# Performance work log

Measured on AMD Instinct MI355X. Metric: run time of the kernel, lower is better.

Reference implementation:

```python
import jax, jax.numpy as jnp
import numpy as np

N_NODES = 50000
N_EDGES = 500000
IN_CH = 128
OUT_CH = 64
HEADS = 4


def setup_inputs() -> dict:
    key = jax.random.key(0)
    ks = jax.random.split(key, 9)
    x = jax.random.normal(ks[0], (N_NODES, IN_CH), dtype=jnp.float32)
    edge_index = jax.random.randint(ks[1], (2, N_EDGES), 0, N_NODES, dtype=jnp.int64)
    edge_weights = jax.random.uniform(ks[2], (N_EDGES, 1), dtype=jnp.float32)
    # xavier-uniform params, stored as [in, out] so y = x @ W
    def xavier(k, shape):
        fan_in, fan_out = shape
        lim = float(np.sqrt(6.0 / (fan_in + fan_out)))
        return jax.random.uniform(k, shape, minval=-lim, maxval=lim, dtype=jnp.float32)
    Wq = xavier(ks[3], (IN_CH, OUT_CH * HEADS))
    Wk = xavier(ks[4], (IN_CH, OUT_CH * HEADS))
    Wv = xavier(ks[5], (IN_CH, OUT_CH * HEADS))
    We = xavier(ks[6], (1, HEADS))
    Wout = xavier(ks[7], (OUT_CH * HEADS, OUT_CH))
    b_out = jnp.zeros((OUT_CH,), dtype=jnp.float32)
    return {"x": x, "edge_index": edge_index, "edge_weights": edge_weights,
            "Wq": Wq, "Wk": Wk, "Wv": Wv, "We": We, "Wout": Wout, "b_out": b_out}


def reference(x, edge_index, edge_weights, Wq, Wk, Wv, We, Wout, b_out):
    num_nodes = x.shape[0]
    src = edge_index[0]
    tgt = edge_index[1]
    x_src = x[src]                                    # [E, in]
    x_tgt = x[tgt]                                    # [E, in]
    q = (x_tgt @ Wq).reshape(-1, HEADS, OUT_CH)       # [E, H, C]
    k = (x_src @ Wk).reshape(-1, HEADS, OUT_CH)
    v = (x_src @ Wv).reshape(-1, HEADS, OUT_CH)
    attn = jnp.sum(q * k, axis=-1) / jnp.sqrt(jnp.float32(OUT_CH))  # [E, H]
    attn = attn + edge_weights @ We                   # [E, H]
    attn = jax.nn.leaky_relu(attn, negative_slope=0.2)
    attn = jax.nn.softmax(attn, axis=0)               # global softmax over edges (as in source)
    weighted_v = attn[..., None] * v                  # [E, H, C]
    out = jax.ops.segment_sum(weighted_v, tgt, num_segments=num_nodes)  # [N, H, C]
    out = out.reshape(num_nodes, HEADS * OUT_CH) @ Wout + b_out         # [N, out]
    if x.shape == out.shape:
        out = out + x
    return out
```

## Files before the change

### kernel.cpp

```cpp
#include <hip/hip_runtime.h>
#include <hip/hip_bf16.h>
#include <hip/hip_fp16.h>

#define N_NODES 50000
#define N_EDGES 500000
#define IN_CH   128
#define D       256
#define UDIM    512
#define OUT_CH  64
#define HEADS   4
#define NC      49
#define PCAP    448
#define DEPTH   4

#define NB_X16  6250
#define NB_HIST 1954
#define NB_MB   256
#define NB_ZB   128
#define NB_GEMM 1564
#define NB_SCAT 1954
#define NB_K4   (NB_GEMM + NB_SCAT)

typedef _Float16 half8 __attribute__((ext_vector_type(8)));
typedef _Float16 half2_t __attribute__((ext_vector_type(2)));
typedef float   floatx4 __attribute__((ext_vector_type(4)));

typedef __attribute__((address_space(1))) const void as1_void;
typedef __attribute__((address_space(3))) void as3_void;

__device__ __forceinline__ void gll16(const void* g, void* l) {
    __builtin_amdgcn_global_load_lds((as1_void*)g, (as3_void*)l, 16, 0, 0);
}

__device__ __forceinline__ float dpp_xor1(float x) {
    return __int_as_float(__builtin_amdgcn_mov_dpp(__float_as_int(x), 0xB1, 0xf, 0xf, true));
}
__device__ __forceinline__ float dpp_xor2(float x) {
    return __int_as_float(__builtin_amdgcn_mov_dpp(__float_as_int(x), 0x4E, 0xf, 0xf, true));
}

__global__ __launch_bounds__(256) void k1_prep_kernel(const float* __restrict__ x,
                                                      __half* __restrict__ x16,
                                                      const int* __restrict__ ei,
                                                      int* __restrict__ cnt,
                                                      double* __restrict__ S,
                                                      const float* __restrict__ Wq,
                                                      const float* __restrict__ Wk,
                                                      const float* __restrict__ Wv,
                                                      const float* __restrict__ Wout,
                                                      __half* __restrict__ M16t,
                                                      __half* __restrict__ Zc16t) {
    __shared__ float sbuf[4][64];
    const int b = blockIdx.x, tid = threadIdx.x;
    if (b < NB_X16) {
        int i = b * 256 + tid;
        if (i < HEADS) S[i] = 0.0;
        int k = i * 4;
        if (k < N_NODES * IN_CH) {
            float4 v = *(const float4*)(x + k);
            union { __half2 h[2]; uint2 u; } pk;
            pk.h[0] = __floats2half2_rn(v.x, v.y);
            pk.h[1] = __floats2half2_rn(v.z, v.w);
            *(uint2*)(x16 + k) = pk.u;
        }
    } else if (b < NB_X16 + NB_HIST) {
        int e = (b - NB_X16) * 256 + tid;
        if (e < N_EDGES) atomicAdd(&cnt[ei[N_EDGES + e]], 1);
    } else if (b < NB_X16 + NB_HIST + NB_MB) {
        const int r = (b - NB_X16 - NB_HIST) * 2 + (tid >> 7);
        const int i = tid & 127;
        const int h = r >> 7, j = r & 127;
        float* buf = sbuf[tid >> 7];
        if (i < 64) buf[i] = Wk[(size_t)j * D + h * 64 + i];
        __syncthreads();
        const float4* qr = (const float4*)(Wq + (size_t)i * D + h * 64);
        float s = 0.f;
        #pragma unroll
        for (int c4 = 0; c4 < 16; ++c4) {
            float4 q = qr[c4];
            s += q.x * buf[c4 * 4] + q.y * buf[c4 * 4 + 1]
               + q.z * buf[c4 * 4 + 2] + q.w * buf[c4 * 4 + 3];
        }
        M16t[(size_t)r * IN_CH + i] = __float2half(s);
    } else {
        const int r = (b - NB_X16 - NB_HIST - NB_MB) * 4 + (tid >> 6);
        const int c = tid & 63;
        const int h = r >> 7, i = r & 127;
        float* buf = sbuf[tid >> 6];
        buf[c] = Wv[(size_t)i * D + h * 64 + c];
        __syncthreads();
        float s = 0.f;
        #pragma unroll 8
        for (int j = 0; j < 64; ++j)
            s += buf[j] * Wout[(size_t)(h * 64 + j) * OUT_CH + c];
        Zc16t[(size_t)c * UDIM + r] = __float2half(s);
    }
}

__global__ __launch_bounds__(256) void k2_scan_reduce_kernel(const int* __restrict__ cnt,
                                                             int* __restrict__ csum) {
    const int b = blockIdx.x, tid = threadIdx.x;
    const int lane = tid & 63, wid = tid >> 6;
    int s = 0;
    int idx0 = b * 1024 + tid * 4;
    #pragma unroll
    for (int i = 0; i < 4; ++i) {
        int idx = idx0 + i;
        if (idx < N_NODES) s += cnt[idx];
    }
    #pragma unroll
    for (int m = 1; m < 64; m <<= 1) s += __shfl_xor(s, m, 64);
    __shared__ int w4[4];
    if (lane == 0) w4[wid] = s;
    __syncthreads();
    if (tid == 0) csum[b] = w4[0] + w4[1] + w4[2] + w4[3];
}

__global__ __launch_bounds__(256) void k3_scan_chunks_kernel(int* __restrict__ cnt,
                                                             const int* __restrict__ csum,
                                                             int* __restrict__ rp) {
    __shared__ int stop[64];
    __shared__ int wsum[4];
    const int b = blockIdx.x, tid = threadIdx.x;
    const int lane = tid & 63, wid = tid >> 6;
    if (tid < 64) stop[tid] = (tid < NC) ? csum[tid] : 0;
    __syncthreads();
    int base = 0;
    for (int w = 0; w < b; ++w) base += stop[w];
    int v[4];
    const int idx0 = b * 1024 + tid * 4;
    #pragma unroll
    for (int i = 0; i < 4; ++i) {
        int idx = idx0 + i;
        v[i] = (idx < N_NODES) ? cnt[idx] : 0;
    }
    int tsum = v[0] + v[1] + v[2] + v[3];
    int x = tsum;
    #pragma unroll
    for (int d = 1; d < 64; d <<= 1) {
        int y = __shfl_up(x, d, 64);
        if (lane >= d) x += y;
    }
    if (lane == 63) wsum[wid] = x;
    __syncthreads();
    int woff = 0;
    for (int w = 0; w < wid; ++w) woff += wsum[w];
    int excl = base + woff + x - tsum;
    #pragma unroll
    for (int i = 0; i < 4; ++i) {
        int idx = idx0 + i;
        if (idx < N_NODES) { rp[idx] = excl; cnt[idx] = excl; }
        excl += v[i];
    }
}

__global__ __launch_bounds__(256) void k4_gemmu_scatter_kernel(const __half* __restrict__ x16,
                                                               const __half* __restrict__ M16t,
                                                               __half* __restrict__ u16,
                                                               const int* __restrict__ ei,
                                                               const float* __restrict__ ew,
                                                               int* __restrict__ cnt,
                                                               int2* __restrict__ payload) {
    __shared__ __half Bm[128][136];
    const int tid = threadIdx.x;
    const int b = blockIdx.x;
    const int glo = (int)(((long long)b * NB_GEMM) / NB_K4);
    const int ghi = (int)(((long long)(b + 1) * NB_GEMM) / NB_K4);
    if (ghi == glo) {
        int e = (b - glo) * 256 + tid;
        if (e < N_EDGES) {
            int s = ei[e], t = ei[N_EDGES + e];
            int pos = atomicAdd(&cnt[t], 1);
            payload[pos] = make_int2(s, __float_as_int(ew[e]));
        }
        return;
    }
    const int m0 = (glo % 391) * 128;
    const int colbase = (glo / 391) * 128;
    {
        const int r = tid >> 1, part = tid & 1;
        const uint4* sb = (const uint4*)(M16t + (size_t)(colbase + r) * IN_CH + part * 64);
        uint4* db = (uint4*)&Bm[r][part * 64];
        #pragma unroll
        for (int q = 0; q < 8; ++q) db[q] = sb[q];
    }

    const int w = tid >> 6, lane = tid & 63;
    const int mrow = lane & 15, quad = lane >> 4;

    half8 a[2][4];
    #pragma unroll
    for (int mt = 0; mt < 2; ++mt) {
        int row = min(m0 + w * 32 + mt * 16 + mrow, N_NODES - 1);
        const __half* ab = x16 + (size_t)row * IN_CH + quad * 8;
        #pragma unroll
        for (int ks = 0; ks < 4; ++ks) a[mt][ks] = *(const half8*)(ab + ks * 32);
    }
    __syncthreads();

    floatx4 acc[2][8];
    #pragma unroll
    for (int mt = 0; mt < 2; ++mt)
        #pragma unroll
        for (int nt = 0; nt < 8; ++nt)
            acc[mt][nt] = (floatx4){0.f, 0.f, 0.f, 0.f};

    #pragma unroll
    for (int nt = 0; nt < 8; ++nt) {
        #pragma unroll
        for (int ks = 0; ks < 4; ++ks) {
            half8 bfr = *(const half8*)&Bm[nt * 16 + mrow][ks * 32 + quad * 8];
            acc[0][nt] = __builtin_amdgcn_mfma_f32_16x16x32_f16(a[0][ks], bfr, acc[0][nt], 0, 0, 0);
            acc[1][nt] = __builtin_amdgcn_mfma_f32_16x16x32_f16(a[1][ks], bfr, acc[1][nt], 0, 0, 0);
        }
    }
    __syncthreads();
    #pragma unroll
    for (int mt = 0; mt < 2; ++mt)
        #pragma unroll
        for (int nt = 0; nt < 8; ++nt)
            #pragma unroll
            for (int r = 0; r < 4; ++r)
                Bm[w * 32 + mt * 16 + quad * 4 + r][nt * 16 + mrow] = __float2half(acc[mt][nt][r]);
    __syncthreads();
    {
        const int r = tid >> 1, part = tid & 1;
        if (m0 + r < N_NODES) {
            const uint4* s4 = (const uint4*)&Bm[r][part * 64];
            uint4* d4 = (uint4*)(u16 + (size_t)(m0 + r) * UDIM + colbase + part * 64);
            #pragma unroll
            for (int q = 0; q < 8; ++q) d4[q] = s4[q];
        }
    }
}

__global__ __launch_bounds__(256) void edge_fused_kernel(const __half* __restrict__ u16,
                                                         const __half* __restrict__ x16,
                                                         const int* __restrict__ rp,
                                                         const int* __restrict__ cnt,
                                                         const int2* __restrict__ payload,
                                                         const float* __restrict__ We,
                                                         __half* __restrict__ y16,
                                                         double* __restrict__ S) {
    __shared__ __half xring[4][DEPTH][512];
    __shared__ int2 pbuf[PCAP];
    __shared__ float sblk[4];
    const int tid = threadIdx.x;
    const int nodebase = blockIdx.x * 16;

    const int span0 = rp[nodebase];
    const int span1 = cnt[nodebase + 15];
    const int span  = span1 - span0;
    const int span_len = min(span, PCAP);
    for (int i = tid; i < span_len; i += 256) pbuf[i] = payload[span0 + i];
    if (tid < 4) sblk[tid] = 0.f;
    __syncthreads();

    const int w = tid >> 6, lane = tid & 63;
    const int g = lane >> 4;
    const int l16 = lane & 15;
    const int h = l16 >> 2;
    const int q = l16 & 3;
    const int node = nodebase + (tid >> 4);
    const float wev = We[h];

    uint4 ur4[4];
    {
        const uint4* ub = (const uint4*)(u16 + (size_t)node * UDIM + h * 128 + q * 32);
        ur4[0] = ub[0]; ur4[1] = ub[1]; ur4[2] = ub[2]; ur4[3] = ub[3];
    }
    const half2_t* uh = (const half2_t*)ur4;

    half2_t yacc[16];
    #pragma unroll
    for (int t = 0; t < 16; ++t) yacc[t] = (half2_t){(_Float16)0.f, (_Float16)0.f};

    float sacc = 0.f;
    const int start = rp[node];
    const int end = cnt[node];
    const int ng = end - start;

    if (span <= PCAP) {
        int nmax = ng;
        nmax = max(nmax, __shfl_xor(nmax, 16, 64));
        nmax = max(nmax, __shfl_xor(nmax, 32, 64));
        if (nmax > 0) {
            const int chunk_off = (l16 ^ g) * 8;
            auto src_of = [&](int t) -> const __half* {
                int idx = min(start + t, end - 1);
                idx = max(idx, span0);
                int s = pbuf[idx - span0].x;
                return x16 + (size_t)s * IN_CH + chunk_off;
            };
            #pragma unroll
            for (int s = 0; s < DEPTH; ++s)
                gll16(src_of(s), &xring[w][s][0]);

            for (int t = 0; t < nmax; ++t) {
                const int slot = t & (DEPTH - 1);
                asm volatile("s_waitcnt vmcnt(3)" ::: "memory");
                __builtin_amdgcn_sched_barrier(0);
                const uint4* rb = (const uint4*)&xring[w][slot][g * 128 + q * 32];
                uint4 xr0 = rb[0 ^ g];
                uint4 xr1 = rb[1 ^ g];
                uint4 xr2 = rb[2 ^ g];
                uint4 xr3 = rb[3 ^ g];
                asm volatile("s_waitcnt lgkmcnt(0)" ::: "memory");
                __builtin_amdgcn_sched_barrier(0);
                gll16(src_of(t + DEPTH), &xring[w][slot][0]);

                int2 pl;
                {
                    int idx = min(start + t, end - 1);
                    idx = max(idx, span0);
                    pl = pbuf[idx - span0];
                }
                uint4 xr[4] = {xr0, xr1, xr2, xr3};
                const half2_t* xh = (const half2_t*)xr;
                float d0 = 0.f, d1 = 0.f, d2 = 0.f, d3 = 0.f;
                #pragma unroll
                for (int tt = 0; tt < 4; ++tt) {
                    d0 = __builtin_amdgcn_fdot2(uh[tt],      xh[tt],      d0, false);
                    d1 = __builtin_amdgcn_fdot2(uh[tt + 4],  xh[tt + 4],  d1, false);
                    d2 = __builtin_amdgcn_fdot2(uh[tt + 8],  xh[tt + 8],  d2, false);
                    d3 = __builtin_amdgcn_fdot2(uh[tt + 12], xh[tt + 12], d3, false);
                }
                float dot = (d0 + d1) + (d2 + d3);
                dot += dpp_xor1(dot);
                dot += dpp_xor2(dot);
                float l = dot * 0.125f + __int_as_float(pl.y) * wev;
                l = fmaxf(l, 0.2f * l);
                float p = __expf(l);
                if (t < ng) {
                    if (q == 0) sacc += p;
                    half2_t p2 = (half2_t){(_Float16)p, (_Float16)p};
                    #pragma unroll
                    for (int tt = 0; tt < 16; ++tt)
                        yacc[tt] = p2 * xh[tt] + yacc[tt];
                }
            }
        }
    } else {
        auto getpl = [&](int e) -> int2 {
            int idx = e - span0;
            return (idx < PCAP) ? pbuf[idx] : payload[e];
        };
        int2 pl = make_int2(0, 0);
        uint4 xr[4];
        if (start < end) {
            pl = getpl(start);
            const uint4* xb = (const uint4*)(x16 + (size_t)pl.x * IN_CH + q * 32);
            xr[0] = xb[0]; xr[1] = xb[1]; xr[2] = xb[2]; xr[3] = xb[3];
        }
        for (int e = start; e < end; ++e) {
            int2 pln = pl;
            uint4 xrn[4] = {xr[0], xr[1], xr[2], xr[3]};
            if (e + 1 < end) {
                pln = getpl(e + 1);
                const uint4* xb = (const uint4*)(x16 + (size_t)pln.x * IN_CH + q * 32);
                xrn[0] = xb[0]; xrn[1] = xb[1]; xrn[2] = xb[2]; xrn[3] = xb[3];
            }
            const half2_t* xh = (const half2_t*)xr;
            float dot = 0.f;
            #pragma unroll
            for (int t = 0; t < 16; ++t)
                dot = __builtin_amdgcn_fdot2(uh[t], xh[t], dot, false);
            dot += __shfl_xor(dot, 1, 16);
            dot += __shfl_xor(dot, 2, 16);
            float l = dot * 0.125f + __int_as_float(pl.y) * wev;
            l = fmaxf(l, 0.2f * l);
            float p = __expf(l);
            if (q == 0) sacc += p;
            half2_t p2 = (half2_t){(_Float16)p, (_Float16)p};
            #pragma unroll
            for (int t = 0; t < 16; ++t)
                yacc[t] = p2 * xh[t] + yacc[t];
            pl = pln;
            xr[0] = xrn[0]; xr[1] = xrn[1]; xr[2] = xrn[2]; xr[3] = xrn[3];
        }
    }
    {
        uint4* yo = (uint4*)(y16 + (size_t)node * UDIM + h * 128 + q * 32);
        const uint4* ys = (const uint4*)yacc;
        yo[0] = ys[0]; yo[1] = ys[1]; yo[2] = ys[2]; yo[3] = ys[3];
    }
    __syncthreads();
    if (q == 0) atomicAdd(&sblk[h], sacc);
    __syncthreads();
    if (tid < 4) atomicAdd(&S[tid], (double)sblk[tid]);
}

__global__ __launch_bounds__(256) void gemm_out_mfma_kernel(const __half* __restrict__ y16,
                                                            const __half* __restrict__ Zc16t,
                                                            const double* __restrict__ S,
                                                            const float* __restrict__ b_out,
                                                            float* __restrict__ out) {
    __shared__ __half Ay[128][136];
    __shared__ __half Bz[64][136];
    __shared__ float invs_s[4];
    const int m0 = blockIdx.x * 128;
    const int tid = threadIdx.x;
    if (tid < 4) invs_s[tid] = (float)(1.0 / S[tid]);

    const int w = tid >> 6, lane = tid & 63;
    const int mrow = lane & 15, quad = lane >> 4;

    floatx4 result[2][4];
    #pragma unroll
    for (int mt = 0; mt < 2; ++mt)
        #pragma unroll
        for (int nt = 0; nt < 4; ++nt)
            result[mt][nt] = (floatx4){0.f, 0.f, 0.f, 0.f};

    for (int h = 0; h < HEADS; ++h) {
        {
            const int r = tid >> 1, part = tid & 1;
            uint4 va[8];
            if (m0 + r < N_NODES) {
                const uint4* src = (const uint4*)(y16 + (size_t)(m0 + r) * UDIM + h * 128 + part * 64);
                #pragma unroll
                for (int qq = 0; qq < 8; ++qq) va[qq] = src[qq];
            } else {
                #pragma unroll
                for (int qq = 0; qq < 8; ++qq) va[qq] = make_uint4(0u, 0u, 0u, 0u);
            }
            uint4* da = (uint4*)&Ay[r][part * 64];
            #pragma unroll
            for (int qq = 0; qq < 8; ++qq) da[qq] = va[qq];
        }
        {
            const int r = tid >> 2, part = tid & 3;
            const uint4* sb = (const uint4*)(Zc16t + (size_t)r * UDIM + h * 128 + part * 32);
            uint4* db = (uint4*)&Bz[r][part * 32];
            #pragma unroll
            for (int qq = 0; qq < 4; ++qq) db[qq] = sb[qq];
        }
        __syncthreads();

        half8 a[2][4];
        #pragma unroll
        for (int mt = 0; mt < 2; ++mt)
            #pragma unroll
            for (int ks = 0; ks < 4; ++ks)
                a[mt][ks] = *(const half8*)&Ay[w * 32 + mt * 16 + mrow][ks * 32 + quad * 8];

        floatx4 acc[2][4];
        #pragma unroll
        for (int mt = 0; mt < 2; ++mt)
            #pragma unroll
            for (int nt = 0; nt < 4; ++nt)
                acc[mt][nt] = (floatx4){0.f, 0.f, 0.f, 0.f};

        #pragma unroll
        for (int nt = 0; nt < 4; ++nt) {
            #pragma unroll
            for (int ks = 0; ks < 4; ++ks) {
                half8 bfr = *(const half8*)&Bz[nt * 16 + mrow][ks * 32 + quad * 8];
                acc[0][nt] = __builtin_amdgcn_mfma_f32_16x16x32_f16(a[0][ks], bfr, acc[0][nt], 0, 0, 0);
                acc[1][nt] = __builtin_amdgcn_mfma_f32_16x16x32_f16(a[1][ks], bfr, acc[1][nt], 0, 0, 0);
            }
        }
        const float inv = invs_s[h];
        #pragma unroll
        for (int mt = 0; mt < 2; ++mt)
            #pragma unroll
            for (int nt = 0; nt < 4; ++nt) {
                result[mt][nt][0] += inv * acc[mt][nt][0];
                result[mt][nt][1] += inv * acc[mt][nt][1];
                result[mt][nt][2] += inv * acc[mt][nt][2];
                result[mt][nt][3] += inv * acc[mt][nt][3];
            }
        __syncthreads();
    }
    float bcol[4];
    #pragma unroll
    for (int nt = 0; nt < 4; ++nt) bcol[nt] = b_out[nt * 16 + mrow];
    #pragma unroll
    for (int mt = 0; mt < 2; ++mt) {
        #pragma unroll
        for (int r = 0; r < 4; ++r) {
            int row = m0 + w * 32 + mt * 16 + quad * 4 + r;
            if (row < N_NODES) {
                float* dst = out + (size_t)row * OUT_CH;
                #pragma unroll
                for (int nt = 0; nt < 4; ++nt)
                    dst[nt * 16 + mrow] = result[mt][nt][r] + bcol[nt];
            }
        }
    }
}

extern "C" void kernel_launch(void* const* d_in, const int* in_sizes, int n_in,
                              void* d_out, int out_size, void* d_ws, size_t ws_size,
                              hipStream_t stream) {
    const float* x     = (const float*)d_in[0];
    const int*   ei    = (const int*)d_in[1];
    const float* ew    = (const float*)d_in[2];
    const float* Wq    = (const float*)d_in[3];
    const float* Wk    = (const float*)d_in[4];
    const float* Wv    = (const float*)d_in[5];
    const float* We    = (const float*)d_in[6];
    const float* Wout  = (const float*)d_in[7];
    const float* b_out = (const float*)d_in[8];
    float* out = (float*)d_out;

    __half* u16   = (__half*)d_ws;
    __half* y16   = u16 + (size_t)N_NODES * UDIM;
    __half* x16   = y16 + (size_t)N_NODES * UDIM;
    double* S     = (double*)(x16 + (size_t)N_NODES * IN_CH);
    __half* M16t  = (__half*)(S + HEADS);
    __half* Zc16t = M16t + UDIM * IN_CH;
    int*    rp    = (int*)(Zc16t + OUT_CH * UDIM);
    int*    cnt   = rp + N_NODES;
    int*    csum  = cnt + N_NODES;
    int2*   payload = (int2*)(csum + 64);

    hipMemsetAsync(cnt, 0, N_NODES * sizeof(int), stream);
    k1_prep_kernel<<<NB_X16 + NB_HIST + NB_MB + NB_ZB, 256, 0, stream>>>(
        x, x16, ei, cnt, S, Wq, Wk, Wv, Wout, M16t, Zc16t);
    k2_scan_reduce_kernel<<<NC, 256, 0, stream>>>(cnt, csum);
    k3_scan_chunks_kernel<<<NC, 256, 0, stream>>>(cnt, csum, rp);
    k4_gemmu_scatter_kernel<<<NB_K4, 256, 0, stream>>>(
        x16, M16t, u16, ei, ew, cnt, payload);
    edge_fused_kernel<<<N_NODES / 16, 256, 0, stream>>>(u16, x16, rp, cnt, payload, We, y16, S);
    gemm_out_mfma_kernel<<<(N_NODES + 127) / 128, 256, 0, stream>>>(y16, Zc16t, S, b_out, out);
}
```

Before: 235.6 us.

## Fuse per-node u projection GEMM into edge kernel via LDS

```diff
diff --git a/kernel.cpp b/kernel.cpp
--- a/kernel.cpp
+++ b/kernel.cpp
@@ -17,9 +17,7 @@
 #define NB_HIST 1954
 #define NB_MB   256
 #define NB_ZB   128
-#define NB_GEMM 1564
 #define NB_SCAT 1954
-#define NB_K4   (NB_GEMM + NB_SCAT)
 
 typedef _Float16 half8 __attribute__((ext_vector_type(8)));
 typedef _Float16 half2_t __attribute__((ext_vector_type(2)));
@@ -154,119 +152,79 @@
     }
 }
 
-__global__ __launch_bounds__(256) void k4_gemmu_scatter_kernel(const __half* __restrict__ x16,
-                                                               const __half* __restrict__ M16t,
-                                                               __half* __restrict__ u16,
-                                                               const int* __restrict__ ei,
-                                                               const float* __restrict__ ew,
-                                                               int* __restrict__ cnt,
-                                                               int2* __restrict__ payload) {
-    __shared__ __half Bm[128][136];
-    const int tid = threadIdx.x;
-    const int b = blockIdx.x;
-    const int glo = (int)(((long long)b * NB_GEMM) / NB_K4);
-    const int ghi = (int)(((long long)(b + 1) * NB_GEMM) / NB_K4);
-    if (ghi == glo) {
-        int e = (b - glo) * 256 + tid;
-        if (e < N_EDGES) {
-            int s = ei[e], t = ei[N_EDGES + e];
-            int pos = atomicAdd(&cnt[t], 1);
-            payload[pos] = make_int2(s, __float_as_int(ew[e]));
-        }
-        return;
-    }
-    const int m0 = (glo % 391) * 128;
-    const int colbase = (glo / 391) * 128;
-    {
-        const int r = tid >> 1, part = tid & 1;
-        const uint4* sb = (const uint4*)(M16t + (size_t)(colbase + r) * IN_CH + part * 64);
-        uint4* db = (uint4*)&Bm[r][part * 64];
-        #pragma unroll
-        for (int q = 0; q < 8; ++q) db[q] = sb[q];
-    }
-
-    const int w = tid >> 6, lane = tid & 63;
-    const int mrow = lane & 15, quad = lane >> 4;
-
-    half8 a[2][4];
-    #pragma unroll
-    for (int mt = 0; mt < 2; ++mt) {
-        int row = min(m0 + w * 32 + mt * 16 + mrow, N_NODES - 1);
-        const __half* ab = x16 + (size_t)row * IN_CH + quad * 8;
-        #pragma unroll
-        for (int ks = 0; ks < 4; ++ks) a[mt][ks] = *(const half8*)(ab + ks * 32);
-    }
-    __syncthreads();
-
-    floatx4 acc[2][8];
-    #pragma unroll
-    for (int mt = 0; mt < 2; ++mt)
-        #pragma unroll
-        for (int nt = 0; nt < 8; ++nt)
-            acc[mt][nt] = (floatx4){0.f, 0.f, 0.f, 0.f};
-
-    #pragma unroll
-    for (int nt = 0; nt < 8; ++nt) {
-        #pragma unroll
-        for (int ks = 0; ks < 4; ++ks) {
-            half8 bfr = *(const half8*)&Bm[nt * 16 + mrow][ks * 32 + quad * 8];
-            acc[0][nt] = __builtin_amdgcn_mfma_f32_16x16x32_f16(a[0][ks], bfr, acc[0][nt], 0, 0, 0);
-            acc[1][nt] = __builtin_amdgcn_mfma_f32_16x16x32_f16(a[1][ks], bfr, acc[1][nt], 0, 0, 0);
-        }
-    }
-    __syncthreads();
-    #pragma unroll
-    for (int mt = 0; mt < 2; ++mt)
-        #pragma unroll
-        for (int nt = 0; nt < 8; ++nt)
-            #pragma unroll
-            for (int r = 0; r < 4; ++r)
-                Bm[w * 32 + mt * 16 + quad * 4 + r][nt * 16 + mrow] = __float2half(acc[mt][nt][r]);
-    __syncthreads();
-    {
-        const int r = tid >> 1, part = tid & 1;
-        if (m0 + r < N_NODES) {
-            const uint4* s4 = (const uint4*)&Bm[r][part * 64];
-            uint4* d4 = (uint4*)(u16 + (size_t)(m0 + r) * UDIM + colbase + part * 64);
-            #pragma unroll
-            for (int q = 0; q < 8; ++q) d4[q] = s4[q];
-        }
-    }
-}
-
-__global__ __launch_bounds__(256) void edge_fused_kernel(const __half* __restrict__ u16,
-                                                         const __half* __restrict__ x16,
-                                                         const int* __restrict__ rp,
-                                                         const int* __restrict__ cnt,
-                                                         const int2* __restrict__ payload,
-                                                         const float* __restrict__ We,
-                                                         __half* __restrict__ y16,
-                                                         double* __restrict__ S) {
+__global__ __launch_bounds__(256) void k4b_scatter_kernel(const int* __restrict__ ei,
+                                                          const float* __restrict__ ew,
+                                                          int* __restrict__ cnt,
+                                                          int2* __restrict__ payload) {
+    int e = blockIdx.x * 256 + threadIdx.x;
+    if (e < N_EDGES) {
+        int s = ei[e], t = ei[N_EDGES + e];
+        int pos = atomicAdd(&cnt[t], 1);
+        payload[pos] = make_int2(s, __float_as_int(ew[e]));
+    }
+}
+
+__global__ __launch_bounds__(256) void fused_ue_kernel(const __half* __restrict__ x16,
+                                                       const __half* __restrict__ M16t,
+                                                       const int* __restrict__ rp,
+                                                       const int* __restrict__ cnt,
+                                                       const int2* __restrict__ payload,
+                                                       const float* __restrict__ We,
+                                                       __half* __restrict__ y16,
+                                                       double* __restrict__ S) {
+    __shared__ __half u_lds[16][520];
     __shared__ __half xring[4][DEPTH][512];
     __shared__ int2 pbuf[PCAP];
     __shared__ float sblk[4];
     const int tid = threadIdx.x;
-    const int nodebase = blockIdx.x * 16;
-
-    const int span0 = rp[nodebase];
-    const int span1 = cnt[nodebase + 15];
+    const int nb0 = blockIdx.x * 16;
+
+    const int span0 = rp[nb0];
+    const int span1 = cnt[nb0 + 15];
     const int span  = span1 - span0;
     const int span_len = min(span, PCAP);
     for (int i = tid; i < span_len; i += 256) pbuf[i] = payload[span0 + i];
     if (tid < 4) sblk[tid] = 0.f;
-    __syncthreads();
 
     const int w = tid >> 6, lane = tid & 63;
+    const int mrow = lane & 15, quad = lane >> 4;
+
+    {
+        half8 a[4];
+        const __half* ab = x16 + (size_t)(nb0 + mrow) * IN_CH + quad * 8;
+        #pragma unroll
+        for (int ks = 0; ks < 4; ++ks) a[ks] = *(const half8*)(ab + ks * 32);
+
+        floatx4 acc[8];
+        #pragma unroll
+        for (int nt = 0; nt < 8; ++nt) acc[nt] = (floatx4){0.f, 0.f, 0.f, 0.f};
+        #pragma unroll
+        for (int nt = 0; nt < 8; ++nt) {
+            const __half* bb = M16t + (size_t)(w * 128 + nt * 16 + mrow) * IN_CH + quad * 8;
+            #pragma unroll
+            for (int ks = 0; ks < 4; ++ks) {
+                half8 bfr = *(const half8*)(bb + ks * 32);
+                acc[nt] = __builtin_amdgcn_mfma_f32_16x16x32_f16(a[ks], bfr, acc[nt], 0, 0, 0);
+            }
+        }
+        #pragma unroll
+        for (int nt = 0; nt < 8; ++nt)
+            #pragma unroll
+            for (int r = 0; r < 4; ++r)
+                u_lds[quad * 4 + r][w * 128 + nt * 16 + mrow] = __float2half(acc[nt][r]);
+    }
+    __syncthreads();
+
     const int g = lane >> 4;
     const int l16 = lane & 15;
     const int h = l16 >> 2;
     const int q = l16 & 3;
-    const int node = nodebase + (tid >> 4);
+    const int node = nb0 + (tid >> 4);
     const float wev = We[h];
 
     uint4 ur4[4];
     {
-        const uint4* ub = (const uint4*)(u16 + (size_t)node * UDIM + h * 128 + q * 32);
+        const uint4* ub = (const uint4*)&u_lds[tid >> 4][h * 128 + q * 32];
         ur4[0] = ub[0]; ur4[1] = ub[1]; ur4[2] = ub[2]; ur4[3] = ub[3];
     }
     const half2_t* uh = (const half2_t*)ur4;
@@ -520,8 +478,7 @@
         x, x16, ei, cnt, S, Wq, Wk, Wv, Wout, M16t, Zc16t);
     k2_scan_reduce_kernel<<<NC, 256, 0, stream>>>(cnt, csum);
     k3_scan_chunks_kernel<<<NC, 256, 0, stream>>>(cnt, csum, rp);
-    k4_gemmu_scatter_kernel<<<NB_K4, 256, 0, stream>>>(
-        x16, M16t, u16, ei, ew, cnt, payload);
-    edge_fused_kernel<<<N_NODES / 16, 256, 0, stream>>>(u16, x16, rp, cnt, payload, We, y16, S);
+    k4b_scatter_kernel<<<NB_SCAT, 256, 0, stream>>>(ei, ew, cnt, payload);
+    fused_ue_kernel<<<N_NODES / 16, 256, 0, stream>>>(x16, M16t, rp, cnt, payload, We, y16, S);
     gemm_out_mfma_kernel<<<(N_NODES + 127) / 128, 256, 0, stream>>>(y16, Zc16t, S, b_out, out);
 }
```

Result: slower. 412.2 us (+75.0%).
